# Performance work log

Hardware: AMD Instinct MI355X
Metric: run time of the kernel (lower is better)

## Reference

```python
import jax, jax.numpy as jnp
import numpy as np

GAMMA = 0.9          # EMA momentum for prototype update
N_CLASSES = 201      # 200 classes + 1 background
K_PROTO = 5          # prototypes per class
FG_THRESH = 0.5      # pca_fg_threshold
SK_EPS = 0.05        # sinkhorn temperature (SwAV-style)
SK_ITERS = 3         # sinkhorn iterations
PCA_ITERS = 10       # niter of torch.pca_lowrank


def _l2norm(x, axis=-1):
    return x / jnp.maximum(jnp.linalg.norm(x, axis=axis, keepdims=True), 1e-12)


def _pca_first_component(X, key):
    # Randomized power iteration for the top left singular vector of the
    # centered data (mirrors torch.pca_lowrank(X, q=1, center=True, niter=10)).
    Xc = X - X.mean(0, keepdims=True)            # [N, D]
    G = Xc.T @ Xc                                # [D, D]
    v = jax.random.normal(key, (X.shape[1],), X.dtype)
    v = v / jnp.linalg.norm(v)
    def body(v, _):
        v = G @ v
        return v / jnp.maximum(jnp.linalg.norm(v), 1e-12), None
    v, _ = jax.lax.scan(body, v, None, length=PCA_ITERS)
    u = Xc @ v                                   # [N]
    return u / jnp.maximum(jnp.linalg.norm(u), 1e-12)


def _masked_sinkhorn(logits, mask):
    # logits: [C, BN, K], mask: [C, BN] bool (rows belonging to class c).
    # Vectorized equivalent of the per-class sinkhorn_knopp(L_c): returns a
    # row-stochastic assignment on the masked rows, balanced over the K cols.
    tiny = 1e-9
    m = mask[..., None].astype(logits.dtype)     # [C, BN, 1]
    Q = jnp.exp(logits / SK_EPS) * m
    n_c = jnp.maximum(mask.sum(-1).astype(logits.dtype), 1.0)[:, None, None]
    K = Q.shape[-1]
    Q = Q / jnp.maximum(Q.sum((-2, -1), keepdims=True), tiny)
    for _ in range(SK_ITERS):
        Q = Q / jnp.maximum(Q.sum(-2, keepdims=True), tiny) / K   # balance cols
        Q = Q * m
        Q = Q / jnp.maximum(Q.sum(-1, keepdims=True), tiny) / n_c # balance rows
        Q = Q * m
    return Q * n_c  # each masked row sums to 1


def setup_inputs() -> dict:
    key = jax.random.key(0)
    k1, k2, k3 = jax.random.split(key, 3)
    B, n_patches, dim = 32, 1024, 768
    patch_tokens = jax.random.normal(k1, (B, n_patches, dim), jnp.float32)
    prototypes = 0.02 * jax.random.normal(k2, (N_CLASSES, K_PROTO, dim), jnp.float32)
    labels = jax.random.randint(k3, (B,), 0, 200).astype(jnp.int64)
    return {"patch_tokens": patch_tokens, "prototypes": prototypes, "labels": labels}


def reference(patch_tokens, prototypes, labels):
    B, n_patches, D = patch_tokens.shape

    pt_norm = _l2norm(patch_tokens)              # [B, N, D]
    proto_norm = _l2norm(prototypes)             # [C, K, D]
    # B n_patches dim, C K dim -> B n_patches C K
    logits = jnp.einsum('bnd,ckd->bnck', pt_norm, proto_norm)

    # ---- get_pseudo_patch_labels (PCA foreground extraction) ----
    X = patch_tokens.reshape(-1, D)
    U = _pca_first_component(X, jax.random.key(1))
    U_scaled = (U - U.min()) / (U.max() - U.min())
    fg = (U_scaled < FG_THRESH).reshape(B, n_patches)
    patch_labels = jnp.where(fg, labels[:, None], N_CLASSES - 1)  # [B, N] int

    # ---- update_prototypes, vectorized over the 201-class python loop ----
    pl_flat = patch_labels.reshape(-1)                            # [B*N]
    L = jnp.transpose(logits.reshape(-1, N_CLASSES, K_PROTO), (1, 0, 2))  # [C, BN, K]
    class_ids = jnp.arange(N_CLASSES)
    mask = pl_flat[None, :] == class_ids[:, None]                 # [C, BN]
    Q = _masked_sinkhorn(L, mask)                                 # [C, BN, K]
    # P_c_new = L_c_assignment.T @ I_c, batched over classes
    P_new = jnp.einsum('cnk,nd->ckd', Q, pt_norm.reshape(-1, D))  # [C, K, D]
    present = (labels[None, :] == class_ids[:, None]).any(-1)     # 'c in labels'
    ema = GAMMA * prototypes + (1.0 - GAMMA) * P_new              # momentum_update
    new_prototypes = jnp.where(present[:, None, None], ema, prototypes)

    image_prototype_logits = logits.max(1)        # [B, C, K]
    class_logits = image_prototype_logits.sum(-1) # [B, C]
    return class_logits, image_prototype_logits, new_prototypes
```

## Files before the change

### kernel.cpp

```cpp
#include <hip/hip_runtime.h>
#include <stdint.h>
#include <stddef.h>

#define DEV static __device__ __forceinline__

typedef __attribute__((ext_vector_type(8))) short bf16x8;
typedef __attribute__((ext_vector_type(4))) float f32x4;
typedef __attribute__((ext_vector_type(4))) int i32x4;

DEV float bf2f(unsigned short u){ union{unsigned int i; float f;} v; v.i = ((unsigned int)u)<<16; return v.f; }
DEV unsigned short f2bf(float f){ union{float f; unsigned int i;} v; v.f=f; unsigned int i=v.i;
  return (unsigned short)((i + 0x7FFFu + ((i>>16)&1u)) >> 16); }
DEV unsigned int fenc(float x){ unsigned int i = __float_as_uint(x); return (i & 0x80000000u) ? ~i : (i | 0x80000000u); }
DEV float fdec(unsigned int e){ unsigned int i = (e & 0x80000000u) ? (e & 0x7FFFFFFFu) : ~e; return __uint_as_float(i); }

DEV float waveSum(float s){
  for (int m=32;m;m>>=1) s += __shfl_xor(s, m, 64);
  return s;
}

DEV float blockSum(float v, float* red){
  int t = threadIdx.x;
  red[t] = v; __syncthreads();
  for (int k=128;k>0;k>>=1){ if (t<k) red[t] += red[t+k]; __syncthreads(); }
  float r = red[0]; __syncthreads();
  return r;
}

DEV void gl16(const void* g, void* lds){
  __builtin_amdgcn_global_load_lds(
      (const __attribute__((address_space(1))) void*)g,
      (__attribute__((address_space(3))) void*)lds, 16, 0, 0);
}

DEV float erfinv_f(float x){
  float w = -log1pf(-__fmul_rn(x,x));
  float p;
  if (w < 5.0f){
    w = w - 2.5f;
    p = 2.81022636e-08f;
    p = 3.43273939e-07f + p*w;
    p = -3.5233877e-06f + p*w;
    p = -4.39150654e-06f + p*w;
    p = 0.00021858087f + p*w;
    p = -0.00125372503f + p*w;
    p = -0.00417768164f + p*w;
    p = 0.246640727f + p*w;
    p = 1.50140941f + p*w;
  } else {
    w = sqrtf(w) - 3.0f;
    p = -0.000200214257f;
    p = 0.000100950558f + p*w;
    p = 0.00134934322f + p*w;
    p = -0.00367342844f + p*w;
    p = 0.00573950773f + p*w;
    p = -0.0076224613f + p*w;
    p = 0.00943887047f + p*w;
    p = 1.00167406f + p*w;
    p = 2.83297682f + p*w;
  }
  return p*x;
}

#define BN_TOT 32768
#define DIM 768
#define NCLS 201
#define KP 5
#define CKPAD 1024
#define NSPLIT_G 16
#define GSPLIT 32
#define PSPLIT 8
#define NBLK_G 672


__global__ void k_setup(unsigned int* ipl_enc, int* cnt, int* cur, int* present,
                        unsigned int* minmax, float* meansum,
                        const int* __restrict__ raw, int* __restrict__ lab,
                        float* __restrict__ v,
                        const float* __restrict__ protos, unsigned short* __restrict__ protn,
                        int* __restrict__ dcnt){
  int i = blockIdx.x*256 + threadIdx.x;
  ipl_enc[i] = 0u;
  if (i < NCLS){ cnt[i]=0; cur[i]=0; present[i]=0; }
  if (i < DIM) meansum[i] = 0.f;
  if (i == 0){
    minmax[0]=0xFFFFFFFFu; minmax[1]=0u;
    dcnt[0] = 0;
    bool is64 = true;
    for (int j=0;j<8;j++){
      int lo = raw[2*j], hi = raw[2*j+1];
      if (hi != 0 || lo < 0 || lo >= NCLS-1){ is64 = false; break; }
    }
    for (int j=0;j<32;j++) lab[j] = is64 ? raw[2*j] : raw[j];
  }
  if (i < DIM){
    unsigned int ks[3] = {0u, 1u, 0x1BD11BDBu};
    const int rot0[4] = {13,15,26,6};
    const int rot1[4] = {17,29,16,24};
    unsigned int x0 = 0u, x1 = (unsigned int)i;
    x0 += ks[0]; x1 += ks[1];
    #pragma unroll
    for (int g=0; g<5; g++){
      const int* rr = (g&1) ? rot1 : rot0;
      #pragma unroll
      for (int j=0;j<4;j++){
        x0 += x1;
        x1 = (x1 << rr[j]) | (x1 >> (32-rr[j]));
        x1 ^= x0;
      }
      x0 += ks[(g+1)%3];
      x1 += ks[(g+2)%3] + (unsigned int)(g+1);
    }
    unsigned int b = x0 ^ x1;
    const float lo = __uint_as_float(0xBF7FFFFFu);
    const float sq2 = __uint_as_float(0x3FB504F3u);
    float f = __uint_as_float((b>>9) | 0x3F800000u) - 1.0f;
    float uu = __fadd_rn(__fmul_rn(f, 2.0f), lo);
    uu = fmaxf(lo, uu);
    v[i] = sq2 * erfinv_f(uu);
  }
  int l = threadIdx.x & 63;
  #pragma unroll
  for (int rr=0; rr<2; rr++){
    int row = blockIdx.x*8 + (threadIdx.x>>6)*2 + rr;
    if (row >= NCLS*KP){
      for (int j=0;j<12;j++) protn[(size_t)row*DIM + l + j*64] = 0;
    } else {
      const float* p = protos + (size_t)row*DIM;
      float x[12]; float s = 0.f;
      for (int j=0;j<12;j++){ x[j] = p[l + j*64]; s += x[j]*x[j]; }
      s = waveSum(s);
      float inv = 1.0f / fmaxf(sqrtf(s), 1e-12f);
      for (int j=0;j<12;j++) protn[(size_t)row*DIM + l + j*64] = f2bf(x[j]*inv);
    }
  }
}

__global__ __launch_bounds__(256) void k_prep(const float* __restrict__ X,
                                              unsigned short* __restrict__ ptn,
                                              signed char* __restrict__ q1T,
                                              signed char* __restrict__ q2T,
                                              float* __restrict__ meansum){
  __shared__ float tile[16][DIM];
  int bid = blockIdx.x;
  int xcd = bid & 7, j = bid >> 3;
  int n0 = xcd*4096 + j*16;
  int t = threadIdx.x;
  {
    const float4* src = (const float4*)(X + (size_t)n0*DIM);
    float4* dst = (float4*)&tile[0][0];
    #pragma unroll
    for (int i=0;i<12;i++) dst[t + i*256] = src[t + i*256];
  }
  __syncthreads();
  int w = t>>6, l = t&63;
  #pragma unroll
  for (int rr=0; rr<4; rr++){
    int r = w*4 + rr;
    const float4* xr = (const float4*)&tile[r][0];
    float4 x4[3]; float s = 0.f;
    #pragma unroll
    for (int jj=0;jj<3;jj++){
      x4[jj] = xr[l + jj*64];
      s += x4[jj].x*x4[jj].x + x4[jj].y*x4[jj].y + x4[jj].z*x4[jj].z + x4[jj].w*x4[jj].w;
    }
    s = waveSum(s);
    float inv = 1.0f / fmaxf(sqrtf(s), 1e-12f);
    #pragma unroll
    for (int jj=0;jj<3;jj++){
      ushort4 o;
      o.x = f2bf(x4[jj].x*inv); o.y = f2bf(x4[jj].y*inv);
      o.z = f2bf(x4[jj].z*inv); o.w = f2bf(x4[jj].w*inv);
      *(ushort4*)&ptn[(size_t)(n0+r)*DIM + 4*(l + jj*64)] = o;
    }
  }
  #pragma unroll
  for (int cc=0; cc<3; cc++){
    int c = t + cc*256;
    unsigned int u1[4], u2[4];
    #pragma unroll
    for (int g=0; g<4; g++){
      unsigned int p1 = 0, p2 = 0;
      #pragma unroll
      for (int k=0;k<4;k++){
        float xx = tile[g*4+k][c];
        int v1 = (int)rintf(xx*16.0f);
        v1 = max(-127, min(127, v1));
        float r2 = xx - (float)v1*(1.0f/16.0f);
        int v2 = (int)rintf(r2*2048.0f);
        v2 = max(-127, min(127, v2));
        p1 |= ((unsigned int)(v1 & 0xff)) << (8*k);
        p2 |= ((unsigned int)(v2 & 0xff)) << (8*k);
      }
      u1[g] = p1; u2[g] = p2;
    }
    uint4 a; a.x=u1[0]; a.y=u1[1]; a.z=u1[2]; a.w=u1[3];
    uint4 b; b.x=u2[0]; b.y=u2[1]; b.z=u2[2]; b.w=u2[3];
    *(uint4*)&q1T[(size_t)c*BN_TOT + n0] = a;
    *(uint4*)&q2T[(size_t)c*BN_TOT + n0] = b;
    float s = 0.f;
    #pragma unroll
    for (int r=0;r<16;r++) s += tile[r][c];
    atomicAdd(&meansum[c], s);
  }
}

DEV void g_coords(int b, int& s, int& ib, int& jb){
  int xcd = b & 7, q = b >> 3;
  s = xcd + 8*(q/21);
  int p = q % 21;
  ib = 0; int rem = p;
  while (rem >= 6 - ib){ rem -= 6 - ib; ib++; }
  jb = ib + rem;
}

__global__ __launch_bounds__(256) void k_mega(const signed char* __restrict__ q1T,
                                              const signed char* __restrict__ q2T,
                                              float* __restrict__ Gpart,
                                              const unsigned short* __restrict__ A,
                                              const unsigned short* __restrict__ Bt,
                                              unsigned int* __restrict__ ipl_enc){
  __shared__ __align__(16) signed char LB[32768];
  __shared__ float red[2][2][64];
  int bid = blockIdx.x;
  int t = threadIdx.x, w = t>>6, l = t&63;
  int wr = w>>1, wc = w&1;

  if (bid < NBLK_G){
    int chain2 = (bid >= 21*NSPLIT_G);
    int s, ib, jb; g_coords(chain2 ? bid - 21*NSPLIT_G : bid, s, ib, jb);
    size_t baseA = (size_t)(ib*128)*BN_TOT;
    size_t baseB = (size_t)(jb*128)*BN_TOT;

    i32x4 acc[4][4];
    #pragma unroll
    for (int m=0;m<4;m++)
      #pragma unroll
      for (int n=0;n<4;n++){ acc[m][n][0]=0; acc[m][n][1]=0; acc[m][n][2]=0; acc[m][n][3]=0; }

    float scale;
    if (!chain2){
      signed char* A1 = LB;
      signed char* B1 = LB + 16384;
      int gu = (l&7) ^ ((l>>3)&7);
      size_t lane_off = (size_t)(l>>3)*BN_TOT + (size_t)gu*16;
      for (int kt=0; kt<16; kt++){
        size_t k0 = (size_t)s*2048 + (size_t)kt*128;
        __syncthreads();
        #pragma unroll
        for (int ci=0; ci<4; ci++){
          int rg = w + ci*4;
          size_t roff = (size_t)(rg*8)*BN_TOT + k0 + lane_off;
          gl16(q1T + baseA + roff, A1 + rg*1024);
          gl16(q1T + baseB + roff, B1 + rg*1024);
        }
        __syncthreads();
        #pragma unroll
        for (int kk=0; kk<2; kk++){
          int physb = (((kk*4) + (l>>4)) ^ (l&7))*16;
          i32x4 b1[4];
          #pragma unroll
          for (int n=0;n<4;n++) b1[n] = *(const i32x4*)&B1[(wc*64 + n*16 + (l&15))*128 + physb];
          #pragma unroll
          for (int m=0;m<4;m++){
            i32x4 a1 = *(const i32x4*)&A1[(wr*64 + m*16 + (l&15))*128 + physb];
            #pragma unroll
            for (int n=0;n<4;n++)
              acc[m][n] = __builtin_amdgcn_mfma_i32_16x16x64_i8(a1, b1[n], acc[m][n], 0,0,0);
          }
        }
      }
      scale = 1.0f/256.0f;
    } else {
      signed char* A1 = LB;
      signed char* A2 = LB + 8192;
      signed char* B1 = LB + 16384;
      signed char* B2 = LB + 24576;
      int gu = (l&3) ^ ((l>>2)&3) ^ (l>>4);
      size_t lane_off = (size_t)(l>>2)*BN_TOT + (size_t)gu*16;
      int physc = (l>>4) ^ (l&3) ^ ((l>>2)&3);
      int rdA = (wr*64 + (l&15))*64 + physc*16;
      int rdB = (wc*64 + (l&15))*64 + physc*16;
      for (int kt=0; kt<32; kt++){
        size_t k0 = (size_t)s*2048 + (size_t)kt*64;
        __syncthreads();
        #pragma unroll
        for (int ci=0; ci<2; ci++){
          int c = w + ci*4;
          size_t roff = (size_t)(c*16)*BN_TOT + k0 + lane_off;
          gl16(q1T + baseA + roff, A1 + c*1024);
          gl16(q2T + baseA + roff, A2 + c*1024);
          gl16(q1T + baseB + roff, B1 + c*1024);
          gl16(q2T + baseB + roff, B2 + c*1024);
        }
        __syncthreads();
        i32x4 b1[4], b2[4];
        #pragma unroll
        for (int n=0;n<4;n++){
          b1[n] = *(const i32x4*)&B1[rdB + n*1024];
          b2[n] = *(const i32x4*)&B2[rdB + n*1024];
        }
        #pragma unroll
        for (int m=0;m<4;m++){
          i32x4 a1 = *(const i32x4*)&A1[rdA + m*1024];
          i32x4 a2 = *(const i32x4*)&A2[rdA + m*1024];
          #pragma unroll
          for (int n=0;n<4;n++){
            acc[m][n] = __builtin_amdgcn_mfma_i32_16x16x64_i8(a1, b2[n], acc[m][n], 0,0,0);
            acc[m][n] = __builtin_amdgcn_mfma_i32_16x16x64_i8(a2, b1[n], acc[m][n], 0,0,0);
          }
        }
      }
      scale = 1.0f/32768.0f;
    }

    int slice = chain2 ? (NSPLIT_G + s) : s;
    float* out = Gpart + (size_t)slice*DIM*DIM;
    #pragma unroll
    for (int m=0;m<4;m++)
      #pragma unroll
      for (int n=0;n<4;n++)
        #pragma unroll
        for (int r=0;r<4;r++){
          int row = ib*128 + wr*64 + m*16 + (l>>4)*4 + r;
          int col = jb*128 + wc*64 + n*16 + (l&15);
          float val = (float)acc[m][n][r]*scale;
          out[(size_t)row*DIM + col] = val;
          if (ib != jb) out[(size_t)col*DIM + row] = val;
        }
  } else {
    unsigned short* As = (unsigned short*)LB;
    unsigned short* Bs = (unsigned short*)(LB + 16384);
    int flat = bid - NBLK_G;
    int xcd = flat & 7, j = flat >> 3;
    int mb = xcd*32 + (j>>3);
    int nb = j & 7;

    int gu = (l&7) ^ ((l>>3)&7);
    size_t lane_off = (size_t)(l>>3)*DIM + (size_t)gu*8;
    size_t baseA = (size_t)(mb*128)*DIM;
    size_t baseB = (size_t)(nb*128)*DIM;

    f32x4 acc[4][4];
    #pragma unroll
    for (int m=0;m<4;m++)
      #pragma unroll
      for (int n=0;n<4;n++){ acc[m][n][0]=0.f; acc[m][n][1]=0.f; acc[m][n][2]=0.f; acc[m][n][3]=0.f; }

    for (int kt=0; kt<12; kt++){
      size_t k0 = (size_t)kt*64;
      __syncthreads();
      #pragma unroll
      for (int ci=0; ci<4; ci++){
        int rg = w + ci*4;
        size_t roff = (size_t)(rg*8)*DIM + k0 + lane_off;
        gl16(A + baseA + roff, &As[rg*512]);
        gl16(Bt + baseB + roff, &Bs[rg*512]);
      }
      __syncthreads();
      #pragma unroll
      for (int kk=0; kk<2; kk++){
        int physb = (((kk*4) + (l>>4)) ^ (l&7))*8;
        bf16x8 a[4], b[4];
        #pragma unroll
        for (int m=0;m<4;m++) a[m] = *(const bf16x8*)&As[(wr*64 + m*16 + (l&15))*64 + physb];
        #pragma unroll
        for (int n=0;n<4;n++) b[n] = *(const bf16x8*)&Bs[(wc*64 + n*16 + (l&15))*64 + physb];
        #pragma unroll
        for (int m=0;m<4;m++)
          #pragma unroll
          for (int n=0;n<4;n++)
            acc[m][n] = __builtin_amdgcn_mfma_f32_16x16x32_bf16(a[m], b[n], acc[m][n], 0,0,0);
      }
    }
    float vmax[4];
    #pragma unroll
    for (int n=0;n<4;n++){
      float v = -1e30f;
      #pragma unroll
      for (int m=0;m<4;m++)
        #pragma unroll
        for (int r=0;r<4;r++) v = fmaxf(v, acc[m][n][r]);
      v = fmaxf(v, __shfl_xor(v, 16, 64));
      v = fmaxf(v, __shfl_xor(v, 32, 64));
      vmax[n] = v;
    }
    __syncthreads();
    if (l < 16){
      #pragma unroll
      for (int n=0;n<4;n++) red[wc][wr][n*16 + l] = vmax[n];
    }
    __syncthreads();
    if (t < 128){
      int wcc = t>>6, col = t&63;
      float v = fmaxf(red[wcc][0][col], red[wcc][1][col]);
      int gcol = nb*128 + wcc*64 + col;
      if (gcol < NCLS*KP){
        int b = (mb*128) >> 10;
        atomicMax(&ipl_enc[b*CKPAD + gcol], fenc(v));
      }
    }
  }
}

__global__ void k_gfix(const float* __restrict__ Gpart, const float* __restrict__ meansum,
                       float* __restrict__ G){
  int i4 = blockIdx.x*256 + threadIdx.x;
  int i = i4*4;
  int r = i/DIM, c = i%DIM;
  float4 s = make_float4(0.f,0.f,0.f,0.f);
  for (int p=0;p<GSPLIT;p++){
    float4 g = *(const float4*)&Gpart[(size_t)p*DIM*DIM + i];
    s.x += g.x; s.y += g.y; s.z += g.z; s.w += g.w;
  }
  const float invN = 1.0f/32768.0f;
  float mr = meansum[r]*invN;
  float4 mc = *(const float4*)&meansum[c];
  float4 o;
  o.x = s.x*invN - mr*mc.x*invN;
  o.y = s.y*invN - mr*mc.y*invN;
  o.z = s.z*invN - mr*mc.z*invN;
  o.w = s.w*invN - mr*mc.w*invN;
  *(float4*)&G[i] = o;
}

__global__ void k_mv(const float* __restrict__ G, const float* __restrict__ vin,
                     float* __restrict__ vout){
  __shared__ float vs[DIM];
  int t = threadIdx.x;
  for (int i=t;i<DIM;i+=256) vs[i] = vin[i];
  __syncthreads();
  int row = blockIdx.x*4 + (t>>6), l = t&63;
  const float* g = G + (size_t)row*DIM;
  float s = 0.f;
  for (int j=0;j<12;j++) s += g[l + j*64]*vs[l + j*64];
  s = waveSum(s);
  if (l==0) vout[row] = s;
}

__global__ void k_u(const float* __restrict__ X, const float* __restrict__ v,
                    const float* __restrict__ meansum,
                    float* __restrict__ u, unsigned int* __restrict__ minmax){
  __shared__ float vs[DIM];
  __shared__ float red[256];
  __shared__ float smn[4], smx[4];
  int t = threadIdx.x;
  for (int i=t;i<DIM;i+=256) vs[i] = v[i];
  __syncthreads();
  float ps = 0.f;
  for (int i=t;i<DIM;i+=256) ps += meansum[i]*(1.0f/32768.0f)*vs[i];
  float scal = blockSum(ps, red);
  int w = t>>6, l = t&63;
  float mn = 1e30f, mx = -1e30f;
  #pragma unroll
  for (int rr=0; rr<4; rr++){
    int row = blockIdx.x*16 + w*4 + rr;
    const float4* xr = (const float4*)(X + (size_t)row*DIM);
    float s = 0.f;
    #pragma unroll
    for (int j=0;j<3;j++){
      float4 x4 = xr[l + j*64];
      int base = 4*(l + j*64);
      s += x4.x*vs[base] + x4.y*vs[base+1] + x4.z*vs[base+2] + x4.w*vs[base+3];
    }
    s = waveSum(s);
    if (l==0){
      float val = s - scal;
      u[row] = val;
      mn = fminf(mn, val); mx = fmaxf(mx, val);
    }
  }
  if (l==0){ smn[w]=mn; smx[w]=mx; }
  __syncthreads();
  if (t==0){
    for (int k=1;k<4;k++){ mn = fminf(mn, smn[k]); mx = fmaxf(mx, smx[k]); }
    atomicMin(&minmax[0], fenc(mn));
    atomicMax(&minmax[1], fenc(mx));
  }
}

__global__ void k_pl(const float* __restrict__ u, const int* __restrict__ labels,
                     const unsigned int* __restrict__ minmax, int* __restrict__ pl,
                     int* __restrict__ cnt, int* __restrict__ offs,
                     int* __restrict__ present, int* __restrict__ dcnt){
  int n = blockIdx.x*256 + threadIdx.x;
  int t = threadIdx.x;
  float umin = fdec(minmax[0]), umax = fdec(minmax[1]);
  float us = (u[n]-umin)/(umax-umin);
  int c = (us < 0.5f) ? labels[n>>10] : (NCLS-1);
  pl[n] = c;
  if (c < NCLS-1) atomicAdd(&cnt[c], 1);
  __threadfence();
  __shared__ int lastblk;
  if (t == 0) lastblk = (atomicAdd(dcnt, 1) == 127) ? 1 : 0;
  __syncthreads();
  if (lastblk){
    __shared__ int sc[256];
    sc[t] = (t < NCLS-1) ? atomicAdd(&cnt[t], 0) : 0;
    __syncthreads();
    for (int d=1; d<256; d<<=1){
      int v = (t >= d) ? sc[t-d] : 0;
      __syncthreads();
      sc[t] += v;
      __syncthreads();
    }
    if (t < NCLS) offs[t] = (t == 0) ? 0 : sc[t-1];
    if (t < 32) atomicOr(&present[labels[t]], 1);
  }
}

__global__ void k_scatter(const int* __restrict__ pl, const int* __restrict__ offs,
                          int* __restrict__ cur, int* __restrict__ idx){
  int n = blockIdx.x*256 + threadIdx.x;
  int c = pl[n];
  if (c < NCLS-1){
    int p = offs[c] + atomicAdd(&cur[c], 1);
    idx[p] = n;
  }
}

__global__ void k_qlog(const int* __restrict__ idx, const int* __restrict__ offs,
                       const int* __restrict__ pl, const unsigned short* __restrict__ ptn,
                       const unsigned short* __restrict__ protn, float* __restrict__ q){
  int i = blockIdx.x*4 + (threadIdx.x>>6);
  int l = threadIdx.x & 63;
  int total = offs[NCLS-1];
  if (i >= total) return;
  int n = idx[i];
  int c = pl[n];
  const unsigned short* pr = ptn + (size_t)n*DIM;
  float x[12];
  for (int j=0;j<12;j++) x[j] = bf2f(pr[l + j*64]);
  for (int k=0;k<KP;k++){
    const unsigned short* wv = protn + (size_t)(c*KP + k)*DIM;
    float s = 0.f;
    for (int j=0;j<12;j++) s += x[j]*bf2f(wv[l + j*64]);
    s = waveSum(s);
    if (l==0) q[(size_t)i*KP + k] = expf(s*20.0f);
  }
}

__global__ void k_sink(const int* __restrict__ cnt, const int* __restrict__ offs,
                       float* __restrict__ q){
  __shared__ float red[256];
  __shared__ float colf[KP];
  int c = blockIdx.x;
  int nc = cnt[c];
  if (nc == 0) return;
  int n0 = offs[c];
  float* Q = q + (size_t)n0*KP;
  int t = threadIdx.x;
  int tot5 = nc*KP;
  float s = 0.f;
  for (int i=t;i<tot5;i+=256) s += Q[i];
  float total = blockSum(s, red);
  float sc = 1.0f/fmaxf(total, 1e-9f);
  for (int i=t;i<tot5;i+=256) Q[i] *= sc;
  __syncthreads();
  float ncf = (float)nc;
  for (int it=0; it<3; it++){
    float cs[KP] = {0,0,0,0,0};
    for (int i=t;i<nc;i+=256){
      const float* row = Q + (size_t)i*KP;
      #pragma unroll
      for (int k=0;k<KP;k++) cs[k] += row[k];
    }
    for (int k=0;k<KP;k++){
      float v = blockSum(cs[k], red);
      if (t==0) colf[k] = 1.0f/(fmaxf(v,1e-9f)*(float)KP);
    }
    __syncthreads();
    for (int i=t;i<nc;i+=256){
      float* row = Q + (size_t)i*KP;
      float qq[KP]; float rs = 0.f;
      #pragma unroll
      for (int k=0;k<KP;k++){ qq[k] = row[k]*colf[k]; rs += qq[k]; }
      float rf = 1.0f/(fmaxf(rs,1e-9f)*ncf);
      #pragma unroll
      for (int k=0;k<KP;k++) row[k] = qq[k]*rf;
    }
    __syncthreads();
  }
  for (int i=t;i<tot5;i+=256) Q[i] *= ncf;
}

__global__ void k_pnew(const int* __restrict__ cnt, const int* __restrict__ offs,
                       const int* __restrict__ present, const int* __restrict__ idx,
                       const float* __restrict__ q, const unsigned short* __restrict__ ptn,
                       float* __restrict__ P4){
  int c = blockIdx.y, s = blockIdx.x;
  if (!present[c]) return;
  int nc = cnt[c], n0 = offs[c];
  int r0 = n0 + (nc*s)/PSPLIT;
  int r1 = n0 + (nc*(s+1))/PSPLIT;
  int t = threadIdx.x;
  float acc[KP][3];
  #pragma unroll
  for (int k=0;k<KP;k++){ acc[k][0]=0.f; acc[k][1]=0.f; acc[k][2]=0.f; }
  for (int i=r0; i<r1; ++i){
    int n = idx[i];
    float qv[KP];
    #pragma unroll
    for (int k=0;k<KP;k++) qv[k] = q[(size_t)i*KP + k];
    const unsigned short* row = ptn + (size_t)n*DIM;
    #pragma unroll
    for (int j=0;j<3;j++){
      float x = bf2f(row[t + j*256]);
      #pragma unroll
      for (int k=0;k<KP;k++) acc[k][j] += qv[k]*x;
    }
  }
  float* out = P4 + ((size_t)(s*NCLS + c)*KP)*DIM;
  #pragma unroll
  for (int k=0;k<KP;k++)
    #pragma unroll
    for (int j=0;j<3;j++)
      out[(size_t)k*DIM + t + j*256] = acc[k][j];
}

__global__ void k_emafinal(const float* __restrict__ protos, const float* __restrict__ P4,
                           const int* __restrict__ present,
                           const unsigned int* __restrict__ ipl_enc,
                           float* __restrict__ out){
  int bid = blockIdx.x;
  if (bid < 3015){
    int i = bid*256 + threadIdx.x;
    if (i >= NCLS*KP*DIM) return;
    int c = i / (KP*DIM);
    float p = protos[i];
    float* o = out + 32*NCLS + 32*NCLS*KP;
    if (present[c]){
      float s = 0.f;
      #pragma unroll
      for (int sp=0; sp<PSPLIT; sp++) s += P4[(size_t)sp*NCLS*KP*DIM + i];
      o[i] = 0.9f*p + 0.1f*s;
    } else {
      o[i] = p;
    }
  } else {
    int i = (bid-3015)*256 + threadIdx.x;
    if (i < 32*NCLS*KP){
      int b = i / (NCLS*KP), ck = i % (NCLS*KP);
      out[32*NCLS + i] = fdec(ipl_enc[b*CKPAD + ck]);
    }
    if (i < 32*NCLS){
      int b = i / NCLS, c = i % NCLS;
      float s = 0.f;
      #pragma unroll
      for (int k=0;k<KP;k++) s += fdec(ipl_enc[b*CKPAD + c*KP + k]);
      out[b*NCLS + c] = s;
    }
  }
}

extern "C" void kernel_launch(void* const* d_in, const int* in_sizes, int n_in,
                              void* d_out, int out_size, void* d_ws, size_t ws_size,
                              hipStream_t stream){
  (void)in_sizes; (void)n_in; (void)out_size; (void)ws_size;
  const float* X = (const float*)d_in[0];
  const float* protos = (const float*)d_in[1];
  const int* labels_raw = (const int*)d_in[2];
  float* out = (float*)d_out;

  char* w = (char*)d_ws;
  size_t off = 0;
  auto alloc = [&](size_t bytes)->void*{
    void* p = (void*)(w + off);
    off = (off + bytes + 255) & ~(size_t)255;
    return p;
  };
  signed char* q1T      = (signed char*)alloc((size_t)DIM*BN_TOT);
  signed char* q2T      = (signed char*)alloc((size_t)DIM*BN_TOT);
  unsigned short* ptn   = (unsigned short*)alloc((size_t)BN_TOT*DIM*2);
  unsigned short* protn = (unsigned short*)alloc((size_t)CKPAD*DIM*2);
  float* Gpart   = (float*)alloc((size_t)GSPLIT*DIM*DIM*4);
  float* G       = (float*)alloc((size_t)DIM*DIM*4);
  float* meansum = (float*)alloc(DIM*4);
  float* vA      = (float*)alloc(DIM*4);
  float* vB      = (float*)alloc(DIM*4);
  int* cnt       = (int*)alloc(1024);
  int* cur       = (int*)alloc(1024);
  int* offs      = (int*)alloc(1024);
  int* present   = (int*)alloc(1024);
  int* labc      = (int*)alloc(256);
  int* dcnt      = (int*)alloc(256);
  unsigned int* minmax  = (unsigned int*)alloc(256);
  unsigned int* ipl_enc = (unsigned int*)alloc((size_t)32*CKPAD*4);

  char* gb = (char*)Gpart;
  size_t goff = 0;
  auto galloc = [&](size_t bytes)->void*{
    void* p = (void*)(gb + goff);
    goff = (goff + bytes + 255) & ~(size_t)255;
    return p;
  };
  float* u_  = (float*)galloc(BN_TOT*4);
  int* pl_   = (int*)galloc(BN_TOT*4);
  int* idx_  = (int*)galloc(BN_TOT*4);
  float* q_  = (float*)galloc((size_t)BN_TOT*KP*4);
  float* P4_ = (float*)galloc((size_t)PSPLIT*NCLS*KP*DIM*4);

  dim3 b256(256);
  k_setup<<<dim3(128), b256, 0, stream>>>(ipl_enc, cnt, cur, present, minmax, meansum,
                                          labels_raw, labc, vA, protos, protn, dcnt);
  k_prep<<<dim3(2048), b256, 0, stream>>>(X, ptn, q1T, q2T, meansum);
  k_mega<<<dim3(NBLK_G + 2048), b256, 0, stream>>>(q1T, q2T, Gpart, ptn, protn, ipl_enc);
  k_gfix<<<dim3(576), b256, 0, stream>>>(Gpart, meansum, G);
  for (int it=0; it<10; it++){
    float* src = (it&1) ? vB : vA;
    float* dst = (it&1) ? vA : vB;
    k_mv<<<dim3(192), b256, 0, stream>>>(G, src, dst);
  }
  k_u<<<dim3(2048), b256, 0, stream>>>(X, vA, meansum, u_, minmax);
  k_pl<<<dim3(128), b256, 0, stream>>>(u_, labc, minmax, pl_, cnt, offs, present, dcnt);
  k_scatter<<<dim3(128), b256, 0, stream>>>(pl_, offs, cur, idx_);
  k_qlog<<<dim3(8192), b256, 0, stream>>>(idx_, offs, pl_, ptn, protn, q_);
  k_sink<<<dim3(200), b256, 0, stream>>>(cnt, offs, q_);
  k_pnew<<<dim3(PSPLIT,NCLS), b256, 0, stream>>>(cnt, offs, present, idx_, q_, ptn, P4_);
  k_emafinal<<<dim3(3141), b256, 0, stream>>>(protos, P4_, present, ipl_enc, out);
}
```

Before: 443.4 us.

## Fuse per-patch foreground prototype logits into prep kernel, drop k_qlog

Computes the exp-scaled dot products of each normalized patch against its image label's five prototypes inside k_prep, while the row is still in registers. This happens before the foreground mask is known, so the result goes to a dense q_all buffer. k_sink then gathers the rows for each class through idx. This removes the separate k_qlog launch and its re-read of ptn. In exchange it computes logits for every patch, including background ones, and adds per-block label-format detection that reads the raw labels.

```diff
diff --git a/kernel.cpp b/kernel.cpp
--- a/kernel.cpp
+++ b/kernel.cpp
@@ -140,7 +140,10 @@
                                               unsigned short* __restrict__ ptn,
                                               signed char* __restrict__ q1T,
                                               signed char* __restrict__ q2T,
-                                              float* __restrict__ meansum){
+                                              float* __restrict__ meansum,
+                                              const unsigned short* __restrict__ protn,
+                                              const int* __restrict__ raw,
+                                              float* __restrict__ q_all){
   __shared__ float tile[16][DIM];
   int bid = blockIdx.x;
   int xcd = bid & 7, j = bid >> 3;
@@ -152,6 +155,14 @@
     #pragma unroll
     for (int i=0;i<12;i++) dst[t + i*256] = src[t + i*256];
   }
+  bool is64 = true;
+  #pragma unroll
+  for (int jj=0;jj<8;jj++){
+    int lo = raw[2*jj], hi = raw[2*jj+1];
+    if (hi != 0 || lo < 0 || lo >= NCLS-1){ is64 = false; break; }
+  }
+  int img = n0 >> 10;
+  int lab = is64 ? raw[2*img] : raw[img];
   __syncthreads();
   int w = t>>6, l = t&63;
   #pragma unroll
@@ -166,12 +177,28 @@
     }
     s = waveSum(s);
     float inv = 1.0f / fmaxf(sqrtf(s), 1e-12f);
+    float xb[12];
     #pragma unroll
     for (int jj=0;jj<3;jj++){
       ushort4 o;
       o.x = f2bf(x4[jj].x*inv); o.y = f2bf(x4[jj].y*inv);
       o.z = f2bf(x4[jj].z*inv); o.w = f2bf(x4[jj].w*inv);
       *(ushort4*)&ptn[(size_t)(n0+r)*DIM + 4*(l + jj*64)] = o;
+      xb[jj*4+0] = bf2f(o.x); xb[jj*4+1] = bf2f(o.y);
+      xb[jj*4+2] = bf2f(o.z); xb[jj*4+3] = bf2f(o.w);
+    }
+    #pragma unroll
+    for (int k=0;k<KP;k++){
+      const ushort4* wv4 = (const ushort4*)&protn[(size_t)(lab*KP + k)*DIM];
+      float sd = 0.f;
+      #pragma unroll
+      for (int jj=0;jj<3;jj++){
+        ushort4 wv = wv4[l + jj*64];
+        sd += xb[jj*4+0]*bf2f(wv.x) + xb[jj*4+1]*bf2f(wv.y)
+            + xb[jj*4+2]*bf2f(wv.z) + xb[jj*4+3]*bf2f(wv.w);
+      }
+      sd = waveSum(sd);
+      if (l==0) q_all[(size_t)(n0+r)*KP + k] = expf(sd*20.0f);
     }
   }
   #pragma unroll
@@ -519,29 +546,9 @@
   }
 }
 
-__global__ void k_qlog(const int* __restrict__ idx, const int* __restrict__ offs,
-                       const int* __restrict__ pl, const unsigned short* __restrict__ ptn,
-                       const unsigned short* __restrict__ protn, float* __restrict__ q){
-  int i = blockIdx.x*4 + (threadIdx.x>>6);
-  int l = threadIdx.x & 63;
-  int total = offs[NCLS-1];
-  if (i >= total) return;
-  int n = idx[i];
-  int c = pl[n];
-  const unsigned short* pr = ptn + (size_t)n*DIM;
-  float x[12];
-  for (int j=0;j<12;j++) x[j] = bf2f(pr[l + j*64]);
-  for (int k=0;k<KP;k++){
-    const unsigned short* wv = protn + (size_t)(c*KP + k)*DIM;
-    float s = 0.f;
-    for (int j=0;j<12;j++) s += x[j]*bf2f(wv[l + j*64]);
-    s = waveSum(s);
-    if (l==0) q[(size_t)i*KP + k] = expf(s*20.0f);
-  }
-}
-
 __global__ void k_sink(const int* __restrict__ cnt, const int* __restrict__ offs,
-                       float* __restrict__ q){
+                       float* __restrict__ q, const int* __restrict__ idx,
+                       const float* __restrict__ q_all){
   __shared__ float red[256];
   __shared__ float colf[KP];
   int c = blockIdx.x;
@@ -550,6 +557,12 @@
   int n0 = offs[c];
   float* Q = q + (size_t)n0*KP;
   int t = threadIdx.x;
+  for (int i=t;i<nc;i+=256){
+    int n = idx[n0+i];
+    #pragma unroll
+    for (int k=0;k<KP;k++) Q[(size_t)i*KP + k] = q_all[(size_t)n*KP + k];
+  }
+  __syncthreads();
   int tot5 = nc*KP;
   float s = 0.f;
   for (int i=t;i<tot5;i+=256) s += Q[i];
@@ -673,6 +686,7 @@
   signed char* q2T      = (signed char*)alloc((size_t)DIM*BN_TOT);
   unsigned short* ptn   = (unsigned short*)alloc((size_t)BN_TOT*DIM*2);
   unsigned short* protn = (unsigned short*)alloc((size_t)CKPAD*DIM*2);
+  float* q_all   = (float*)alloc((size_t)BN_TOT*KP*4);
   float* Gpart   = (float*)alloc((size_t)GSPLIT*DIM*DIM*4);
   float* G       = (float*)alloc((size_t)DIM*DIM*4);
   float* meansum = (float*)alloc(DIM*4);
@@ -703,7 +717,7 @@
   dim3 b256(256);
   k_setup<<<dim3(128), b256, 0, stream>>>(ipl_enc, cnt, cur, present, minmax, meansum,
                                           labels_raw, labc, vA, protos, protn, dcnt);
-  k_prep<<<dim3(2048), b256, 0, stream>>>(X, ptn, q1T, q2T, meansum);
+  k_prep<<<dim3(2048), b256, 0, stream>>>(X, ptn, q1T, q2T, meansum, protn, labels_raw, q_all);
   k_mega<<<dim3(NBLK_G + 2048), b256, 0, stream>>>(q1T, q2T, Gpart, ptn, protn, ipl_enc);
   k_gfix<<<dim3(576), b256, 0, stream>>>(Gpart, meansum, G);
   for (int it=0; it<10; it++){
@@ -714,8 +728,7 @@
   k_u<<<dim3(2048), b256, 0, stream>>>(X, vA, meansum, u_, minmax);
   k_pl<<<dim3(128), b256, 0, stream>>>(u_, labc, minmax, pl_, cnt, offs, present, dcnt);
   k_scatter<<<dim3(128), b256, 0, stream>>>(pl_, offs, cur, idx_);
-  k_qlog<<<dim3(8192), b256, 0, stream>>>(idx_, offs, pl_, ptn, protn, q_);
-  k_sink<<<dim3(200), b256, 0, stream>>>(cnt, offs, q_);
+  k_sink<<<dim3(200), b256, 0, stream>>>(cnt, offs, q_, idx_, q_all);
   k_pnew<<<dim3(PSPLIT,NCLS), b256, 0, stream>>>(cnt, offs, present, idx_, q_, ptn, P4_);
   k_emafinal<<<dim3(3141), b256, 0, stream>>>(protos, P4_, present, ipl_enc, out);
 }
```

Measured after the change: 450.7 us. Within noise of the previous version (+1.6%).
